# Performance work log

Measured on AMD Instinct MI355X. Metric: run time of the kernel, lower is better.

## Reference

```python
import jax, jax.numpy as jnp
import numpy as np

NU = 0.01 / np.pi  # Burgers viscosity
LAYERS = [2, 128, 128, 128, 128, 1]
N_EQ, N_INIT, N_BND = 131072, 4096, 4096


def setup_inputs() -> dict:
    key = jax.random.key(0)
    ks = jax.random.split(key, 16)
    inp = {
        'tx_equation': jax.random.uniform(ks[0], (N_EQ, 2), dtype=jnp.float32),
        'tx_init': jax.random.uniform(ks[1], (N_INIT, 2), dtype=jnp.float32),
        'tx_bound': jax.random.uniform(ks[2], (N_BND, 2), dtype=jnp.float32),
    }
    # Glorot-normal initialized Dense weights, zero biases (keras defaults in build_network)
    for i, (fin, fout) in enumerate(zip(LAYERS[:-1], LAYERS[1:])):
        std = np.sqrt(2.0 / (fin + fout)).astype(np.float32)
        inp[f'W{i}'] = jax.random.normal(ks[3 + i], (fin, fout), dtype=jnp.float32) * std
        inp[f'b{i}'] = jnp.zeros((fout,), dtype=jnp.float32)
    return inp


def _mlp_scalar(tx, Ws, bs):
    # tx: (2,) -> scalar u. tanh hidden layers, linear output.
    h = tx
    for W, b in zip(Ws[:-1], bs[:-1]):
        h = jnp.tanh(h @ W + b)
    return (h @ Ws[-1] + bs[-1])[0]


def reference(tx_equation, tx_init, tx_bound, W0, b0, W1, b1, W2, b2, W3, b3, W4, b4):
    Ws = [W0, W1, W2, W3, W4]
    bs = [b0, b1, b2, b3, b4]

    def u_s(tx):
        return _mlp_scalar(tx, Ws, bs)

    def u_x_s(tx):
        return jax.grad(u_s)(tx)[1]

    # PDE residual on collocation points
    u = jax.vmap(u_s)(tx_equation)                     # (N,)
    g = jax.vmap(jax.grad(u_s))(tx_equation)           # (N, 2) -> columns (u_t, u_x)
    u_t, u_x = g[:, 0], g[:, 1]
    u_xx = jax.vmap(jax.grad(u_x_s))(tx_equation)[:, 1]  # (N,)
    burgers_eq = (u_t + u * u_x - NU * u_xx)[:, None]     # (N, 1)

    # Initial / boundary predictions (single fused batch like tf.concat in call)
    tx_ib = jnp.concatenate([tx_init, tx_bound], axis=0)
    u_ib = jax.vmap(u_s)(tx_ib)[:, None]
    n_i = tx_init.shape[0]
    return burgers_eq, u_ib[:n_i], u_ib[n_i:]
```

## Files before the change

### kernel.cpp

```cpp
#include <hip/hip_runtime.h>
#include <math.h>

#define NU_F 0.0031830988618379067f
#define HS 136
#define TANH_C 2.8853900817779268f

typedef __attribute__((ext_vector_type(8))) _Float16 half8;
typedef __attribute__((ext_vector_type(4))) _Float16 half4;
typedef __attribute__((ext_vector_type(16))) float f32x16;

__device__ __forceinline__ float fast_tanh(float x) {
    const float e = __builtin_amdgcn_exp2f(x * TANH_C);
    const float r = __builtin_amdgcn_rcpf(e + 1.f);
    return fmaf(-2.f, r, 1.f);
}

__device__ __forceinline__ float fast_tanh_pre(float x, float b2) {
    const float e = __builtin_amdgcn_exp2f(fmaf(x, TANH_C, b2));
    const float r = __builtin_amdgcn_rcpf(e + 1.f);
    return fmaf(-2.f, r, 1.f);
}

__global__ void prep_kernel(const float* __restrict__ W1,
                            const float* __restrict__ W2,
                            const float* __restrict__ W3,
                            _Float16* __restrict__ ws)
{
    const int g = blockIdx.x * 256 + threadIdx.x;
    const int l = g >> 14;
    const int r = g & 16383;
    const int n = r & 127;
    const int k = r >> 7;
    const float* W = (l == 0) ? W1 : (l == 1) ? W2 : W3;
    const float w = W[k * 128 + n];
    ws[l * 16384 + (k >> 4) * 2048 + n * 16 + (k & 15)] = (_Float16)w;
}

__launch_bounds__(256, 4)
__global__ void pinn_kernel(const float* __restrict__ tx_eq,
                            const float* __restrict__ tx_init,
                            const float* __restrict__ tx_bnd,
                            const float* __restrict__ W0, const float* __restrict__ b0,
                            const float* __restrict__ b1, const float* __restrict__ b2,
                            const float* __restrict__ b3,
                            const float* __restrict__ W4, const float* __restrict__ b4,
                            const _Float16* __restrict__ wt,
                            float* __restrict__ out)
{
    __shared__ _Float16 Hh[128][HS];

    const int tid   = threadIdx.x;
    const int blk   = blockIdx.x;
    const bool is_eq = (blk < 4096);
    const int w     = tid >> 6;
    const int lane  = tid & 63;
    const int col   = lane & 31;
    const int khalf = lane >> 5;
    const int ncol  = 32 * w + col;
    const int wofs  = ncol * 16 + khalf * 8;

    float tv, xv;
    if (is_eq) {
        const float2 t2 = ((const float2*)tx_eq)[blk * 32 + (tid >> 3)];
        tv = t2.x; xv = t2.y;
    } else {
        const int p  = tid >> 1;
        const int gp = (blk - 4096) * 128 + p;
        const float2* src = (gp < 4096) ? (const float2*)tx_init : (const float2*)tx_bnd;
        const int idx = (gp < 4096) ? gp : gp - 4096;
        const float2 t2 = src[idx];
        tv = t2.x; xv = t2.y;
    }

    const _Float16* ph = wt + wofs;
    half8 q0 = *(const half8*)(ph);
    half8 q1 = *(const half8*)(ph + 2048);
    half8 q2 = *(const half8*)(ph + 4096);
    half8 q3 = *(const half8*)(ph + 6144);
    half8 q4 = *(const half8*)(ph + 8192);
    half8 q5 = *(const half8*)(ph + 10240);
    half8 q6 = *(const half8*)(ph + 12288);
    half8 q7 = *(const half8*)(ph + 14336);

    f32x16 Z;
    #pragma unroll
    for (int e = 0; e < 16; ++e) Z[e] = 0.f;

    if (is_eq) {
        const int p  = tid >> 3;
        const int f0 = (tid & 7) * 16;
        const int m0 = 4 * p;
        #pragma unroll
        for (int half = 0; half < 2; ++half) {
            const int fb = f0 + 8 * half;
            float vch[4][8];
            #pragma unroll
            for (int j = 0; j < 8; ++j) {
                const int f = fb + j;
                const float w0v = W0[f];
                const float w1v = W0[128 + f];
                const float z = fmaf(tv, w0v, fmaf(xv, w1v, b0[f]));
                const float a = fast_tanh(z);
                const float s = 1.f - a * a;
                const float v2 = s * w1v;
                vch[0][j] = a;
                vch[1][j] = s * w0v;
                vch[2][j] = v2;
                vch[3][j] = ((a * v2) * w1v) * -2.f;
            }
            #pragma unroll
            for (int c = 0; c < 4; ++c) {
                half8 hh;
                #pragma unroll
                for (int j = 0; j < 8; ++j) hh[j] = (_Float16)vch[c][j];
                *(half8*)&Hh[m0 + c][fb] = hh;
            }
        }
    } else {
        const int p  = tid >> 1;
        const int f0 = (tid & 1) * 64;
        #pragma unroll
        for (int g = 0; g < 8; ++g) {
            half8 hh;
            #pragma unroll
            for (int j = 0; j < 8; ++j) {
                const int f = f0 + 8 * g + j;
                hh[j] = (_Float16)fast_tanh(fmaf(tv, W0[f], fmaf(xv, W0[128 + f], b0[f])));
            }
            *(half8*)&Hh[p][f0 + 8 * g] = hh;
        }
    }
    __syncthreads();

    const float* barr[3] = {b1, b2, b3};

    #pragma unroll 1
    for (int layer = 0; layer < 3; ++layer) {
        const float bias2 = barr[layer][ncol] * TANH_C;

        f32x16 acc0, acc1, acc2, acc3;

#define KSTEP0(Q)                                                             \
        {                                                                     \
            const int k0 = khalf * 8;                                         \
            const half8 ah0 = *(const half8*)&Hh[col][k0];                    \
            const half8 ah1 = *(const half8*)&Hh[32 + col][k0];               \
            const half8 ah2 = *(const half8*)&Hh[64 + col][k0];               \
            const half8 ah3 = *(const half8*)&Hh[96 + col][k0];               \
            acc0 = __builtin_amdgcn_mfma_f32_32x32x16_f16(ah0, Q, Z, 0, 0, 0); \
            acc1 = __builtin_amdgcn_mfma_f32_32x32x16_f16(ah1, Q, Z, 0, 0, 0); \
            acc2 = __builtin_amdgcn_mfma_f32_32x32x16_f16(ah2, Q, Z, 0, 0, 0); \
            acc3 = __builtin_amdgcn_mfma_f32_32x32x16_f16(ah3, Q, Z, 0, 0, 0); \
        }
#define KSTEP(KT, Q)                                                          \
        {                                                                     \
            const int k0 = KT * 16 + khalf * 8;                               \
            const half8 ah0 = *(const half8*)&Hh[col][k0];                    \
            const half8 ah1 = *(const half8*)&Hh[32 + col][k0];               \
            const half8 ah2 = *(const half8*)&Hh[64 + col][k0];               \
            const half8 ah3 = *(const half8*)&Hh[96 + col][k0];               \
            acc0 = __builtin_amdgcn_mfma_f32_32x32x16_f16(ah0, Q, acc0, 0, 0, 0); \
            acc1 = __builtin_amdgcn_mfma_f32_32x32x16_f16(ah1, Q, acc1, 0, 0, 0); \
            acc2 = __builtin_amdgcn_mfma_f32_32x32x16_f16(ah2, Q, acc2, 0, 0, 0); \
            acc3 = __builtin_amdgcn_mfma_f32_32x32x16_f16(ah3, Q, acc3, 0, 0, 0); \
        }
        __builtin_amdgcn_s_setprio(1);
        KSTEP0(q0) KSTEP(1, q1) KSTEP(2, q2) KSTEP(3, q3)
        KSTEP(4, q4) KSTEP(5, q5) KSTEP(6, q6) KSTEP(7, q7)
        __builtin_amdgcn_s_setprio(0);
#undef KSTEP0
#undef KSTEP

        if (layer < 2) {
            ph += 16384;
            q0 = *(const half8*)(ph);
            q1 = *(const half8*)(ph + 2048);
            q2 = *(const half8*)(ph + 4096);
            q3 = *(const half8*)(ph + 6144);
            q4 = *(const half8*)(ph + 8192);
            q5 = *(const half8*)(ph + 10240);
            q6 = *(const half8*)(ph + 12288);
            q7 = *(const half8*)(ph + 14336);
        }

        half4 h16[4][4];
        #pragma unroll
        for (int mt = 0; mt < 4; ++mt)
            #pragma unroll
            for (int g = 0; g < 4; ++g) {
                const float A0 = (mt == 0 ? acc0 : mt == 1 ? acc1 : mt == 2 ? acc2 : acc3)[4 * g + 0];
                const float A1 = (mt == 0 ? acc0 : mt == 1 ? acc1 : mt == 2 ? acc2 : acc3)[4 * g + 1];
                const float A2 = (mt == 0 ? acc0 : mt == 1 ? acc1 : mt == 2 ? acc2 : acc3)[4 * g + 2];
                const float A3 = (mt == 0 ? acc0 : mt == 1 ? acc1 : mt == 2 ? acc2 : acc3)[4 * g + 3];
                half4 hv;
                if (is_eq) {
                    const float t = fast_tanh_pre(A0, bias2);
                    const float s = 1.f - t * t;
                    const float sA2 = s * A2;
                    hv[0] = (_Float16)t;
                    hv[1] = (_Float16)(s * A1);
                    hv[2] = (_Float16)sA2;
                    hv[3] = (_Float16)fmaf(s, A3, -2.f * ((t * sA2) * A2));
                } else {
                    hv[0] = (_Float16)fast_tanh_pre(A0, bias2);
                    hv[1] = (_Float16)fast_tanh_pre(A1, bias2);
                    hv[2] = (_Float16)fast_tanh_pre(A2, bias2);
                    hv[3] = (_Float16)fast_tanh_pre(A3, bias2);
                }
                h16[mt][g] = hv;
            }

        __syncthreads();

        #pragma unroll
        for (int mt = 0; mt < 4; ++mt)
            #pragma unroll
            for (int g = 0; g < 4; ++g) {
                const int mrow0 = mt * 32 + 8 * g + 4 * khalf;
                Hh[mrow0 + 0][ncol] = h16[mt][g][0];
                Hh[mrow0 + 1][ncol] = h16[mt][g][1];
                Hh[mrow0 + 2][ncol] = h16[mt][g][2];
                Hh[mrow0 + 3][ncol] = h16[mt][g][3];
            }
        __syncthreads();
    }

    {
        const float b4v = b4[0];
        const int m = tid >> 1;
        const int q = tid & 1;
        float dot = 0.f;
        #pragma unroll
        for (int g = 0; g < 8; ++g) {
            const int f = 64 * q + 8 * g;
            const half8 hh = *(const half8*)&Hh[m][f];
            const float4 wa = *(const float4*)&W4[f];
            const float4 wb = *(const float4*)&W4[f + 4];
            dot = fmaf((float)hh[0], wa.x, dot);
            dot = fmaf((float)hh[1], wa.y, dot);
            dot = fmaf((float)hh[2], wa.z, dot);
            dot = fmaf((float)hh[3], wa.w, dot);
            dot = fmaf((float)hh[4], wb.x, dot);
            dot = fmaf((float)hh[5], wb.y, dot);
            dot = fmaf((float)hh[6], wb.z, dot);
            dot = fmaf((float)hh[7], wb.w, dot);
        }
        dot += __shfl_xor(dot, 1);

        if (is_eq) {
            const int base = (lane & 7) * 8;
            const float uu   = __shfl(dot, base + 0) + b4v;
            const float utv  = __shfl(dot, base + 2);
            const float uxv  = __shfl(dot, base + 4);
            const float uxxv = __shfl(dot, base + 6);
            if (lane < 8)
                out[blk * 32 + 8 * w + lane] = fmaf(uu, uxv, utv) - NU_F * uxxv;
        } else {
            if (q == 0)
                out[131072 + (blk - 4096) * 128 + m] = dot + b4v;
        }
    }
}

extern "C" void kernel_launch(void* const* d_in, const int* in_sizes, int n_in,
                              void* d_out, int out_size, void* d_ws, size_t ws_size,
                              hipStream_t stream)
{
    const float* tx_eq   = (const float*)d_in[0];
    const float* tx_init = (const float*)d_in[1];
    const float* tx_bnd  = (const float*)d_in[2];
    const float* W0 = (const float*)d_in[3];
    const float* b0 = (const float*)d_in[4];
    const float* W1 = (const float*)d_in[5];
    const float* b1 = (const float*)d_in[6];
    const float* W2 = (const float*)d_in[7];
    const float* b2 = (const float*)d_in[8];
    const float* W3 = (const float*)d_in[9];
    const float* b3 = (const float*)d_in[10];
    const float* W4 = (const float*)d_in[11];
    const float* b4 = (const float*)d_in[12];
    float* out = (float*)d_out;
    _Float16* wt = (_Float16*)d_ws;

    hipLaunchKernelGGL(prep_kernel, dim3(192), dim3(256), 0, stream, W1, W2, W3, wt);
    hipLaunchKernelGGL(pinn_kernel, dim3(4160), dim3(256), 0, stream,
                       tx_eq, tx_init, tx_bnd, W0, b0, b1, b2, b3, W4, b4,
                       (const _Float16*)wt, out);
}
```

Measured before the change: 160.0 us.

## Partition hidden layers by row per wave to drop block barriers

Each wave now owns 32 rows of the activation tile instead of 32 output columns. It loads its A fragments once per layer and loops over four N tiles, writing results back to its own rows of shared memory. Since no wave reads another wave's rows, all the `__syncthreads` calls between layers are removed. In exchange, the weights are no longer held in registers and prefetched. Each wave now reloads the full layer's weights from global/L2 for every N tile, which may expose load latency and raise cache traffic.

```diff
diff --git a/kernel.cpp b/kernel.cpp
--- a/kernel.cpp
+++ b/kernel.cpp
@@ -56,8 +56,7 @@
     const int lane  = tid & 63;
     const int col   = lane & 31;
     const int khalf = lane >> 5;
-    const int ncol  = 32 * w + col;
-    const int wofs  = ncol * 16 + khalf * 8;
+    const int rbase = 32 * w;
 
     float tv, xv;
     if (is_eq) {
@@ -71,16 +70,6 @@
         const float2 t2 = src[idx];
         tv = t2.x; xv = t2.y;
     }
-
-    const _Float16* ph = wt + wofs;
-    half8 q0 = *(const half8*)(ph);
-    half8 q1 = *(const half8*)(ph + 2048);
-    half8 q2 = *(const half8*)(ph + 4096);
-    half8 q3 = *(const half8*)(ph + 6144);
-    half8 q4 = *(const half8*)(ph + 8192);
-    half8 q5 = *(const half8*)(ph + 10240);
-    half8 q6 = *(const half8*)(ph + 12288);
-    half8 q7 = *(const half8*)(ph + 14336);
 
     f32x16 Z;
     #pragma unroll
@@ -130,68 +119,56 @@
             *(half8*)&Hh[p][f0 + 8 * g] = hh;
         }
     }
-    __syncthreads();
 
     const float* barr[3] = {b1, b2, b3};
+    const _Float16* wl = wt;
 
     #pragma unroll 1
     for (int layer = 0; layer < 3; ++layer) {
-        const float bias2 = barr[layer][ncol] * TANH_C;
-
-        f32x16 acc0, acc1, acc2, acc3;
-
-#define KSTEP0(Q)                                                             \
-        {                                                                     \
-            const int k0 = khalf * 8;                                         \
-            const half8 ah0 = *(const half8*)&Hh[col][k0];                    \
-            const half8 ah1 = *(const half8*)&Hh[32 + col][k0];               \
-            const half8 ah2 = *(const half8*)&Hh[64 + col][k0];               \
-            const half8 ah3 = *(const half8*)&Hh[96 + col][k0];               \
-            acc0 = __builtin_amdgcn_mfma_f32_32x32x16_f16(ah0, Q, Z, 0, 0, 0); \
-            acc1 = __builtin_amdgcn_mfma_f32_32x32x16_f16(ah1, Q, Z, 0, 0, 0); \
-            acc2 = __builtin_amdgcn_mfma_f32_32x32x16_f16(ah2, Q, Z, 0, 0, 0); \
-            acc3 = __builtin_amdgcn_mfma_f32_32x32x16_f16(ah3, Q, Z, 0, 0, 0); \
-        }
-#define KSTEP(KT, Q)                                                          \
-        {                                                                     \
-            const int k0 = KT * 16 + khalf * 8;                               \
-            const half8 ah0 = *(const half8*)&Hh[col][k0];                    \
-            const half8 ah1 = *(const half8*)&Hh[32 + col][k0];               \
-            const half8 ah2 = *(const half8*)&Hh[64 + col][k0];               \
-            const half8 ah3 = *(const half8*)&Hh[96 + col][k0];               \
-            acc0 = __builtin_amdgcn_mfma_f32_32x32x16_f16(ah0, Q, acc0, 0, 0, 0); \
-            acc1 = __builtin_amdgcn_mfma_f32_32x32x16_f16(ah1, Q, acc1, 0, 0, 0); \
-            acc2 = __builtin_amdgcn_mfma_f32_32x32x16_f16(ah2, Q, acc2, 0, 0, 0); \
-            acc3 = __builtin_amdgcn_mfma_f32_32x32x16_f16(ah3, Q, acc3, 0, 0, 0); \
-        }
-        __builtin_amdgcn_s_setprio(1);
-        KSTEP0(q0) KSTEP(1, q1) KSTEP(2, q2) KSTEP(3, q3)
-        KSTEP(4, q4) KSTEP(5, q5) KSTEP(6, q6) KSTEP(7, q7)
-        __builtin_amdgcn_s_setprio(0);
-#undef KSTEP0
-#undef KSTEP
-
-        if (layer < 2) {
-            ph += 16384;
-            q0 = *(const half8*)(ph);
-            q1 = *(const half8*)(ph + 2048);
-            q2 = *(const half8*)(ph + 4096);
-            q3 = *(const half8*)(ph + 6144);
-            q4 = *(const half8*)(ph + 8192);
-            q5 = *(const half8*)(ph + 10240);
-            q6 = *(const half8*)(ph + 12288);
-            q7 = *(const half8*)(ph + 14336);
-        }
-
-        half4 h16[4][4];
-        #pragma unroll
-        for (int mt = 0; mt < 4; ++mt)
+        const _Float16* ar = &Hh[rbase + col][khalf * 8];
+        const half8 a0 = *(const half8*)(ar);
+        const half8 a1 = *(const half8*)(ar + 16);
+        const half8 a2 = *(const half8*)(ar + 32);
+        const half8 a3 = *(const half8*)(ar + 48);
+        const half8 a4 = *(const half8*)(ar + 64);
+        const half8 a5 = *(const half8*)(ar + 80);
+        const half8 a6 = *(const half8*)(ar + 96);
+        const half8 a7 = *(const half8*)(ar + 112);
+
+        const float* __restrict__ bl = barr[layer];
+
+        #pragma unroll
+        for (int nt = 0; nt < 4; ++nt) {
+            const _Float16* pb = wl + nt * 512 + col * 16 + khalf * 8;
+            const half8 w0_ = *(const half8*)(pb);
+            const half8 w1_ = *(const half8*)(pb + 2048);
+            const half8 w2_ = *(const half8*)(pb + 4096);
+            const half8 w3_ = *(const half8*)(pb + 6144);
+            const half8 w4_ = *(const half8*)(pb + 8192);
+            const half8 w5_ = *(const half8*)(pb + 10240);
+            const half8 w6_ = *(const half8*)(pb + 12288);
+            const half8 w7_ = *(const half8*)(pb + 14336);
+            const float bias2 = bl[32 * nt + col] * TANH_C;
+
+            __builtin_amdgcn_s_setprio(1);
+            f32x16 acc;
+            acc = __builtin_amdgcn_mfma_f32_32x32x16_f16(a0, w0_, Z,   0, 0, 0);
+            acc = __builtin_amdgcn_mfma_f32_32x32x16_f16(a1, w1_, acc, 0, 0, 0);
+            acc = __builtin_amdgcn_mfma_f32_32x32x16_f16(a2, w2_, acc, 0, 0, 0);
+            acc = __builtin_amdgcn_mfma_f32_32x32x16_f16(a3, w3_, acc, 0, 0, 0);
+            acc = __builtin_amdgcn_mfma_f32_32x32x16_f16(a4, w4_, acc, 0, 0, 0);
+            acc = __builtin_amdgcn_mfma_f32_32x32x16_f16(a5, w5_, acc, 0, 0, 0);
+            acc = __builtin_amdgcn_mfma_f32_32x32x16_f16(a6, w6_, acc, 0, 0, 0);
+            acc = __builtin_amdgcn_mfma_f32_32x32x16_f16(a7, w7_, acc, 0, 0, 0);
+            __builtin_amdgcn_s_setprio(0);
+
+            const int nc = 32 * nt + col;
             #pragma unroll
             for (int g = 0; g < 4; ++g) {
-                const float A0 = (mt == 0 ? acc0 : mt == 1 ? acc1 : mt == 2 ? acc2 : acc3)[4 * g + 0];
-                const float A1 = (mt == 0 ? acc0 : mt == 1 ? acc1 : mt == 2 ? acc2 : acc3)[4 * g + 1];
-                const float A2 = (mt == 0 ? acc0 : mt == 1 ? acc1 : mt == 2 ? acc2 : acc3)[4 * g + 2];
-                const float A3 = (mt == 0 ? acc0 : mt == 1 ? acc1 : mt == 2 ? acc2 : acc3)[4 * g + 3];
+                const float A0 = acc[4 * g + 0];
+                const float A1 = acc[4 * g + 1];
+                const float A2 = acc[4 * g + 2];
+                const float A3 = acc[4 * g + 3];
                 half4 hv;
                 if (is_eq) {
                     const float t = fast_tanh_pre(A0, bias2);
@@ -207,22 +184,14 @@
                     hv[2] = (_Float16)fast_tanh_pre(A2, bias2);
                     hv[3] = (_Float16)fast_tanh_pre(A3, bias2);
                 }
-                h16[mt][g] = hv;
-            }
-
-        __syncthreads();
-
-        #pragma unroll
-        for (int mt = 0; mt < 4; ++mt)
-            #pragma unroll
-            for (int g = 0; g < 4; ++g) {
-                const int mrow0 = mt * 32 + 8 * g + 4 * khalf;
-                Hh[mrow0 + 0][ncol] = h16[mt][g][0];
-                Hh[mrow0 + 1][ncol] = h16[mt][g][1];
-                Hh[mrow0 + 2][ncol] = h16[mt][g][2];
-                Hh[mrow0 + 3][ncol] = h16[mt][g][3];
-            }
-        __syncthreads();
+                const int mrow0 = rbase + 8 * g + 4 * khalf;
+                Hh[mrow0 + 0][nc] = hv[0];
+                Hh[mrow0 + 1][nc] = hv[1];
+                Hh[mrow0 + 2][nc] = hv[2];
+                Hh[mrow0 + 3][nc] = hv[3];
+            }
+        }
+        wl += 16384;
     }
 
     {
```

Result: slower. 176.7 us (+10.4%).

## Fuse final hidden layer with output projection via DPP cross-lane reduction

Applied to the files above, without the earlier changes.

Peels the last hidden layer out of the loop and applies the W4 output weights directly in registers. Each 32-column slice is reduced across lanes with DPP row operations and a transpose-style select tree, then written as partial sums to a small shared buffer. This removes the final write of the full hidden state to LDS, one barrier, and the 128-wide dot-product read pass. In exchange it adds many DPP adds and selects per tile (about 64 DPP ops per thread per tile) and extra register pressure.

```diff
diff --git a/kernel.cpp b/kernel.cpp
--- a/kernel.cpp
+++ b/kernel.cpp
@@ -19,6 +19,14 @@
     const float e = __builtin_amdgcn_exp2f(fmaf(x, TANH_C, b2));
     const float r = __builtin_amdgcn_rcpf(e + 1.f);
     return fmaf(-2.f, r, 1.f);
+}
+
+template<int CTRL>
+__device__ __forceinline__ float fdpp(float v) {
+    union { float f; int i; } a, b;
+    a.f = v;
+    b.i = __builtin_amdgcn_update_dpp(0, a.i, CTRL, 0xF, 0xF, true);
+    return b.f;
 }
 
 __global__ void prep_kernel(const float* __restrict__ W1,
@@ -48,6 +56,7 @@
                             float* __restrict__ out)
 {
     __shared__ _Float16 Hh[128][HS];
+    __shared__ float   part[128][8];
 
     const int tid   = threadIdx.x;
     const int blk   = blockIdx.x;
@@ -132,14 +141,6 @@
     }
     __syncthreads();
 
-    const float* barr[3] = {b1, b2, b3};
-
-    #pragma unroll 1
-    for (int layer = 0; layer < 3; ++layer) {
-        const float bias2 = barr[layer][ncol] * TANH_C;
-
-        f32x16 acc0, acc1, acc2, acc3;
-
 #define KSTEP0(Q)                                                             \
         {                                                                     \
             const int k0 = khalf * 8;                                         \
@@ -164,24 +165,27 @@
             acc2 = __builtin_amdgcn_mfma_f32_32x32x16_f16(ah2, Q, acc2, 0, 0, 0); \
             acc3 = __builtin_amdgcn_mfma_f32_32x32x16_f16(ah3, Q, acc3, 0, 0, 0); \
         }
+
+    const float* barr[2] = {b1, b2};
+    #pragma unroll 1
+    for (int layer = 0; layer < 2; ++layer) {
+        const float bias2 = barr[layer][ncol] * TANH_C;
+
+        f32x16 acc0, acc1, acc2, acc3;
         __builtin_amdgcn_s_setprio(1);
         KSTEP0(q0) KSTEP(1, q1) KSTEP(2, q2) KSTEP(3, q3)
         KSTEP(4, q4) KSTEP(5, q5) KSTEP(6, q6) KSTEP(7, q7)
         __builtin_amdgcn_s_setprio(0);
-#undef KSTEP0
-#undef KSTEP
-
-        if (layer < 2) {
-            ph += 16384;
-            q0 = *(const half8*)(ph);
-            q1 = *(const half8*)(ph + 2048);
-            q2 = *(const half8*)(ph + 4096);
-            q3 = *(const half8*)(ph + 6144);
-            q4 = *(const half8*)(ph + 8192);
-            q5 = *(const half8*)(ph + 10240);
-            q6 = *(const half8*)(ph + 12288);
-            q7 = *(const half8*)(ph + 14336);
-        }
+
+        ph += 16384;
+        q0 = *(const half8*)(ph);
+        q1 = *(const half8*)(ph + 2048);
+        q2 = *(const half8*)(ph + 4096);
+        q3 = *(const half8*)(ph + 6144);
+        q4 = *(const half8*)(ph + 8192);
+        q5 = *(const half8*)(ph + 10240);
+        q6 = *(const half8*)(ph + 12288);
+        q7 = *(const half8*)(ph + 14336);
 
         half4 h16[4][4];
         #pragma unroll
@@ -226,25 +230,78 @@
     }
 
     {
+        const float bias2 = b3[ncol] * TANH_C;
+        const float w4c   = W4[ncol];
+
+        f32x16 acc0, acc1, acc2, acc3;
+        __builtin_amdgcn_s_setprio(1);
+        KSTEP0(q0) KSTEP(1, q1) KSTEP(2, q2) KSTEP(3, q3)
+        KSTEP(4, q4) KSTEP(5, q5) KSTEP(6, q6) KSTEP(7, q7)
+        __builtin_amdgcn_s_setprio(0);
+
+        const int  pc    = 2 * w + ((lane >> 4) & 1);
+        const bool lb0   = (lane & 1) != 0;
+        const bool lb1   = (lane & 2) != 0;
+        const bool lb2   = (lane & 4) != 0;
+        const bool lb3   = (lane & 8) != 0;
+        #pragma unroll
+        for (int mt = 0; mt < 4; ++mt) {
+            float p[16];
+            #pragma unroll
+            for (int g = 0; g < 4; ++g) {
+                const float A0 = (mt == 0 ? acc0 : mt == 1 ? acc1 : mt == 2 ? acc2 : acc3)[4 * g + 0];
+                const float A1 = (mt == 0 ? acc0 : mt == 1 ? acc1 : mt == 2 ? acc2 : acc3)[4 * g + 1];
+                const float A2 = (mt == 0 ? acc0 : mt == 1 ? acc1 : mt == 2 ? acc2 : acc3)[4 * g + 2];
+                const float A3 = (mt == 0 ? acc0 : mt == 1 ? acc1 : mt == 2 ? acc2 : acc3)[4 * g + 3];
+                float h0v, h1v, h2v, h3v;
+                if (is_eq) {
+                    const float t = fast_tanh_pre(A0, bias2);
+                    const float s = 1.f - t * t;
+                    const float sA2 = s * A2;
+                    h0v = t;
+                    h1v = s * A1;
+                    h2v = sA2;
+                    h3v = fmaf(s, A3, -2.f * ((t * sA2) * A2));
+                } else {
+                    h0v = fast_tanh_pre(A0, bias2);
+                    h1v = fast_tanh_pre(A1, bias2);
+                    h2v = fast_tanh_pre(A2, bias2);
+                    h3v = fast_tanh_pre(A3, bias2);
+                }
+                p[4 * g + 0] = (float)(_Float16)h0v * w4c;
+                p[4 * g + 1] = (float)(_Float16)h1v * w4c;
+                p[4 * g + 2] = (float)(_Float16)h2v * w4c;
+                p[4 * g + 3] = (float)(_Float16)h3v * w4c;
+            }
+            #pragma unroll
+            for (int i = 0; i < 16; ++i) {
+                p[i] += fdpp<0xB1>(p[i]);
+                p[i] += fdpp<0x4E>(p[i]);
+                p[i] += fdpp<0x124>(p[i]);
+                p[i] += fdpp<0x128>(p[i]);
+            }
+            float t0[8], t1[4], t2[2];
+            #pragma unroll
+            for (int j = 0; j < 8; ++j) t0[j] = lb0 ? p[2 * j + 1] : p[2 * j];
+            #pragma unroll
+            for (int j = 0; j < 4; ++j) t1[j] = lb1 ? t0[2 * j + 1] : t0[2 * j];
+            #pragma unroll
+            for (int j = 0; j < 2; ++j) t2[j] = lb2 ? t1[2 * j + 1] : t1[2 * j];
+            const float v = lb3 ? t2[1] : t2[0];
+            const int row = mt * 32 + 8 * ((lane >> 2) & 3) + 4 * khalf + (lane & 3);
+            part[row][pc] = v;
+        }
+    }
+#undef KSTEP0
+#undef KSTEP
+    __syncthreads();
+
+    {
         const float b4v = b4[0];
         const int m = tid >> 1;
         const int q = tid & 1;
-        float dot = 0.f;
-        #pragma unroll
-        for (int g = 0; g < 8; ++g) {
-            const int f = 64 * q + 8 * g;
-            const half8 hh = *(const half8*)&Hh[m][f];
-            const float4 wa = *(const float4*)&W4[f];
-            const float4 wb = *(const float4*)&W4[f + 4];
-            dot = fmaf((float)hh[0], wa.x, dot);
-            dot = fmaf((float)hh[1], wa.y, dot);
-            dot = fmaf((float)hh[2], wa.z, dot);
-            dot = fmaf((float)hh[3], wa.w, dot);
-            dot = fmaf((float)hh[4], wb.x, dot);
-            dot = fmaf((float)hh[5], wb.y, dot);
-            dot = fmaf((float)hh[6], wb.z, dot);
-            dot = fmaf((float)hh[7], wb.w, dot);
-        }
+        const float4 pv = *(const float4*)&part[m][4 * q];
+        float dot = (pv.x + pv.y) + (pv.z + pv.w);
         dot += __shfl_xor(dot, 1);
 
         if (is_eq) {
```

Result: slower. 203.1 us (+26.9%).
